# Optimization experiments

Measured on AMD Instinct MI355X. Metric: run time of the kernel, lower is better.

Reference implementation:

```python
import jax, jax.numpy as jnp
import numpy as np

NEG = 1e30  # same large negative mask constant as the torch code
E_PAIRS, N_CLASSES, SEG_LEN = 65536, 97, 8
N_ROWS = E_PAIRS * SEG_LEN


def setup_inputs() -> dict:
    key = jax.random.key(0)
    k1, k2 = jax.random.split(key)
    logits = jax.random.normal(k1, (N_ROWS, N_CLASSES), dtype=jnp.float32)
    labels = (jax.random.uniform(k2, (E_PAIRS, N_CLASSES)) < 0.05).astype(jnp.float32)
    # contiguous (st, en) ranges tiling logits rows, pos[0,0] == 0
    starts = jnp.arange(E_PAIRS, dtype=jnp.int32) * SEG_LEN
    pos = jnp.stack([starts, starts + SEG_LEN], axis=1)  # [E, 2]
    return {"logits": logits, "labels": labels, "pos": pos}


def reference(logits, labels, pos):
    E, C = labels.shape
    N = logits.shape[0]
    # pos segments are contiguous starting at pos[0,0] == 0, covering all rows
    lens = pos[:, 1] - pos[:, 0]
    seg_ids = jnp.repeat(jnp.arange(E), lens, total_repeat_length=N)  # [N]

    # ragged segment-max pooling over mention-combination rows
    e_logits = jax.ops.segment_max(logits, seg_ids, num_segments=E)  # [E, C]

    # labels[:, 0] = 0; p_mask = labels + th_label (th_label has 1 in col 0)
    labels = labels.at[:, 0].set(0.0)
    p_mask = labels.at[:, 0].set(1.0)
    n_mask = 1.0 - labels

    # loss1: masked log-softmax over pooled logits, summed over positive labels
    e_logit1 = e_logits - (1.0 - p_mask) * NEG
    loss1 = -(jax.nn.log_softmax(e_logit1, axis=-1) * labels).sum(axis=1)  # [E]

    # loss2: per-row masked log-softmax; n_mask broadcast to each row of its segment
    m_n_mask = n_mask[seg_ids]  # [N, C]
    m_logit2 = logits - (1.0 - m_n_mask) * NEG
    loss2 = -jax.nn.log_softmax(m_logit2, axis=-1)[:, 0]  # th_label selects col 0

    return loss1.mean() + loss2.mean()
```

## Files before the change

kernel.cpp:

```cpp
#include <hip/hip_runtime.h>
#include <math.h>


#define NCLS 97
#define SEGS_PER_WAVE 8
#define WAVES_PER_BLOCK 4

__global__ __launch_bounds__(256) void atloss_stage1(
    const float* __restrict__ logits,
    const float* __restrict__ labels,
    const int*   __restrict__ pos,
    float*       __restrict__ partials,
    int E, float invE, float invN)
{
    const int tid  = threadIdx.x;
    const int wv   = tid >> 6;
    const int lane = tid & 63;
    const int j    = lane & 15;
    const int r    = lane >> 4;
    const int gwave = blockIdx.x * WAVES_PER_BLOCK + wv;

    float acc1 = 0.0f;
    float acc2 = 0.0f;

    #pragma unroll 1
    for (int s = 0; s < SEGS_PER_WAVE; ++s) {
        const int e = gwave * SEGS_PER_WAVE + s;
        if (e < E) {
            const int st = pos[2 * e];
            const float* __restrict__ la = logits + (size_t)(st + r) * NCLS;
            const float* __restrict__ lb = logits + (size_t)(st + r + 4) * NCLS;
            const float* __restrict__ lg = labels + (size_t)e * NCLS;

            unsigned long long mlo = __ballot(lg[lane] > 0.5f) & ~1ull;
            unsigned long long mhi = __ballot((lane < NCLS - 64) ? (lg[64 + lane] > 0.5f)
                                                                 : false);

            float xa[7], xb[7];
            #pragma unroll
            for (int k = 0; k < 6; ++k) {
                xa[k] = la[j + 16 * k];
                xb[k] = lb[j + 16 * k];
            }
            if (j == 0) { xa[6] = la[96]; xb[6] = lb[96]; }
            else        { xa[6] = -INFINITY; xb[6] = -INFINITY; }

            float s2a = 0.0f, s2b = 0.0f;
            float cm[7];
            #pragma unroll
            for (int k = 0; k < 7; ++k) {
                const int c = j + 16 * k;
                const bool pf = (c < 64) ? ((mlo >> c) & 1ull)
                                         : ((mhi >> (c - 64)) & 1ull);
                s2a += pf ? 0.0f : __expf(xa[k]);
                s2b += pf ? 0.0f : __expf(xb[k]);
                cm[k] = fmaxf(xa[k], xb[k]);
            }
            s2a += __shfl_xor(s2a, 1); s2b += __shfl_xor(s2b, 1);
            s2a += __shfl_xor(s2a, 2); s2b += __shfl_xor(s2b, 2);
            s2a += __shfl_xor(s2a, 4); s2b += __shfl_xor(s2b, 4);
            s2a += __shfl_xor(s2a, 8); s2b += __shfl_xor(s2b, 8);
            if (j == 0)
                acc2 += (__logf(s2a) - xa[0]) + (__logf(s2b) - xb[0]);

            #pragma unroll
            for (int k = 0; k < 7; ++k) {
                cm[k] = fmaxf(cm[k], __shfl_xor(cm[k], 16));
                cm[k] = fmaxf(cm[k], __shfl_xor(cm[k], 32));
            }

            float s1 = 0.0f, psum = 0.0f;
            #pragma unroll
            for (int k = 0; k < 7; ++k) {
                const int c = j + 16 * k;
                const bool pf = (c < 64) ? ((mlo >> c) & 1ull)
                                         : ((mhi >> (c - 64)) & 1ull);
                const bool inP = pf || (c == 0);
                s1   += inP ? __expf(cm[k]) : 0.0f;
                psum += pf ? cm[k] : 0.0f;
            }
            s1   += __shfl_xor(s1, 1);   psum += __shfl_xor(psum, 1);
            s1   += __shfl_xor(s1, 2);   psum += __shfl_xor(psum, 2);
            s1   += __shfl_xor(s1, 4);   psum += __shfl_xor(psum, 4);
            s1   += __shfl_xor(s1, 8);   psum += __shfl_xor(psum, 8);
            if (lane == 0) {
                const float pcnt = (float)(__popcll(mlo) + __popcll(mhi));
                acc1 += pcnt * __logf(s1) - psum;
            }
        }
    }

    float tot = acc1 * invE + acc2 * invN;
    tot += __shfl_xor(tot, 16);
    tot += __shfl_xor(tot, 32);

    __shared__ float red[WAVES_PER_BLOCK];
    if (lane == 0) red[wv] = tot;
    __syncthreads();
    if (tid == 0) {
        float b = 0.0f;
        #pragma unroll
        for (int w = 0; w < WAVES_PER_BLOCK; ++w) b += red[w];
        partials[blockIdx.x] = b;
    }
}

__global__ __launch_bounds__(256) void atloss_reduce(
    const float* __restrict__ p, int n, float* __restrict__ out)
{
    float s = 0.0f;
    for (int i = threadIdx.x; i < n; i += 256) s += p[i];
    #pragma unroll
    for (int m = 1; m <= 32; m <<= 1) s += __shfl_xor(s, m);
    __shared__ float red[4];
    if ((threadIdx.x & 63) == 0) red[threadIdx.x >> 6] = s;
    __syncthreads();
    if (threadIdx.x == 0) out[0] = red[0] + red[1] + red[2] + red[3];
}

extern "C" void kernel_launch(void* const* d_in, const int* in_sizes, int n_in,
                              void* d_out, int out_size, void* d_ws, size_t ws_size,
                              hipStream_t stream)
{
    const float* logits = (const float*)d_in[0];
    const float* labels = (const float*)d_in[1];
    const int*   pos    = (const int*)d_in[2];

    const int E     = in_sizes[1] / NCLS;
    const int Nrows = in_sizes[0] / NCLS;

    const int segs_per_block = SEGS_PER_WAVE * WAVES_PER_BLOCK;
    const int nblocks = (E + segs_per_block - 1) / segs_per_block;

    float* partials = (float*)d_ws;

    atloss_stage1<<<nblocks, 256, 0, stream>>>(
        logits, labels, pos, partials, E, 1.0f / (float)E, 1.0f / (float)Nrows);
    atloss_reduce<<<1, 256, 0, stream>>>(partials, nblocks, (float*)d_out);
}
```

Measured before the change: 302.7 us.

## Double-buffer segment loads with register prefetch and batched pos loads

Loads all eight segment start offsets for a wave in one vector load and broadcasts them by shuffle. The per-segment loop becomes a fully unrolled software pipeline: the logits and labels loads for the next segment are issued before the current segment is computed, using two register buffers. This is meant to hide global memory latency in a bandwidth-bound kernel. It raises register pressure and loads out of range for tail segments, which are masked by clamped indices and a validity flag.

```diff
diff --git a/kernel.cpp b/kernel.cpp
--- a/kernel.cpp
+++ b/kernel.cpp
@@ -20,75 +20,103 @@
     const int r    = lane >> 4;
     const int gwave = blockIdx.x * WAVES_PER_BLOCK + wv;
 
+    int ep0 = gwave * SEGS_PER_WAVE + (lane & 7);
+    if (ep0 > E - 1) ep0 = E - 1;
+    const int stl = pos[2 * ep0];
+
     float acc1 = 0.0f;
     float acc2 = 0.0f;
 
-    #pragma unroll 1
-    for (int s = 0; s < SEGS_PER_WAVE; ++s) {
-        const int e = gwave * SEGS_PER_WAVE + s;
-        if (e < E) {
-            const int st = pos[2 * e];
-            const float* __restrict__ la = logits + (size_t)(st + r) * NCLS;
-            const float* __restrict__ lb = logits + (size_t)(st + r + 4) * NCLS;
-            const float* __restrict__ lg = labels + (size_t)e * NCLS;
+    float xaA[7], xbA[7], l0A, l1A;
+    float xaB[7], xbB[7], l0B, l1B;
 
-            unsigned long long mlo = __ballot(lg[lane] > 0.5f) & ~1ull;
-            unsigned long long mhi = __ballot((lane < NCLS - 64) ? (lg[64 + lane] > 0.5f)
-                                                                 : false);
+#define ISSUE(S, XA, XB, L0, L1)                                           \
+    do {                                                                   \
+        const int e_ = gwave * SEGS_PER_WAVE + (S);                        \
+        const int st_ = __shfl(stl, (S));                                  \
+        const float* __restrict__ la_ = logits + (size_t)(st_ + r) * NCLS; \
+        const float* __restrict__ lb_ = la_ + 4 * NCLS;                    \
+        const float* __restrict__ lg_ =                                    \
+            labels + (size_t)(e_ < E ? e_ : 0) * NCLS;                     \
+        _Pragma("unroll")                                                  \
+        for (int k = 0; k < 6; ++k) {                                      \
+            XA[k] = la_[j + 16 * k];                                       \
+            XB[k] = lb_[j + 16 * k];                                       \
+        }                                                                  \
+        XA[6] = la_[96];        \
+        XB[6] = lb_[96];                                                   \
+        L0 = lg_[lane];                                                    \
+        L1 = (lane < NCLS - 64) ? lg_[64 + lane] : 0.0f;                   \
+    } while (0)
 
-            float xa[7], xb[7];
-            #pragma unroll
-            for (int k = 0; k < 6; ++k) {
-                xa[k] = la[j + 16 * k];
-                xb[k] = lb[j + 16 * k];
-            }
-            if (j == 0) { xa[6] = la[96]; xb[6] = lb[96]; }
-            else        { xa[6] = -INFINITY; xb[6] = -INFINITY; }
+#define COMPUTE(S, XA, XB, L0, L1)                                         \
+    do {                                                                   \
+        const bool valid_ = (gwave * SEGS_PER_WAVE + (S)) < E;             \
+           \
+        unsigned long long mlo_ = __ballot(L0 > 0.5f) & ~1ull;             \
+        unsigned long long mhi_ = __ballot(L1 > 0.5f);                     \
+        float va[7], vb[7];                                                \
+        _Pragma("unroll")                                                  \
+        for (int k = 0; k < 6; ++k) { va[k] = XA[k]; vb[k] = XB[k]; }      \
+        va[6] = (j == 0) ? XA[6] : -INFINITY;                              \
+        vb[6] = (j == 0) ? XB[6] : -INFINITY;                              \
+              \
+        float s2a = 0.0f, s2b = 0.0f;                                      \
+        float cm[7];                                                       \
+        _Pragma("unroll")                                                  \
+        for (int k = 0; k < 7; ++k) {                                      \
+            const int c = j + 16 * k;                                      \
+            const bool pf = (c < 64) ? ((mlo_ >> c) & 1ull)                \
+                                     : ((mhi_ >> (c - 64)) & 1ull);        \
+            s2a += pf ? 0.0f : __expf(va[k]);                              \
+            s2b += pf ? 0.0f : __expf(vb[k]);                              \
+            cm[k] = fmaxf(va[k], vb[k]);                                   \
+        }                                                                  \
+        s2a += __shfl_xor(s2a, 1); s2b += __shfl_xor(s2b, 1);              \
+        s2a += __shfl_xor(s2a, 2); s2b += __shfl_xor(s2b, 2);              \
+        s2a += __shfl_xor(s2a, 4); s2b += __shfl_xor(s2b, 4);              \
+        s2a += __shfl_xor(s2a, 8); s2b += __shfl_xor(s2b, 8);              \
+        if (j == 0 && valid_)                                              \
+            acc2 += (__logf(s2a) - va[0]) + (__logf(s2b) - vb[0]);         \
+                      \
+        _Pragma("unroll")                                                  \
+        for (int k = 0; k < 7; ++k) {                                      \
+            cm[k] = fmaxf(cm[k], __shfl_xor(cm[k], 16));                   \
+            cm[k] = fmaxf(cm[k], __shfl_xor(cm[k], 32));                   \
+        }                                                                  \
+             \
+        float s1 = 0.0f, psum = 0.0f;                                      \
+        _Pragma("unroll")                                                  \
+        for (int k = 0; k < 7; ++k) {                                      \
+            const int c = j + 16 * k;                                      \
+            const bool pf = (c < 64) ? ((mlo_ >> c) & 1ull)                \
+                                     : ((mhi_ >> (c - 64)) & 1ull);        \
+            const bool inP = pf || (c == 0);                               \
+            s1   += inP ? __expf(cm[k]) : 0.0f;                            \
+            psum += pf ? cm[k] : 0.0f;                                     \
+        }                                                                  \
+        s1 += __shfl_xor(s1, 1);  psum += __shfl_xor(psum, 1);             \
+        s1 += __shfl_xor(s1, 2);  psum += __shfl_xor(psum, 2);             \
+        s1 += __shfl_xor(s1, 4);  psum += __shfl_xor(psum, 4);             \
+        s1 += __shfl_xor(s1, 8);  psum += __shfl_xor(psum, 8);             \
+        if (lane == 0 && valid_) {                                         \
+            const float pcnt = (float)(__popcll(mlo_) + __popcll(mhi_));   \
+            acc1 += pcnt * __logf(s1) - psum;                              \
+        }                                                                  \
+    } while (0)
 
-            float s2a = 0.0f, s2b = 0.0f;
-            float cm[7];
-            #pragma unroll
-            for (int k = 0; k < 7; ++k) {
-                const int c = j + 16 * k;
-                const bool pf = (c < 64) ? ((mlo >> c) & 1ull)
-                                         : ((mhi >> (c - 64)) & 1ull);
-                s2a += pf ? 0.0f : __expf(xa[k]);
-                s2b += pf ? 0.0f : __expf(xb[k]);
-                cm[k] = fmaxf(xa[k], xb[k]);
-            }
-            s2a += __shfl_xor(s2a, 1); s2b += __shfl_xor(s2b, 1);
-            s2a += __shfl_xor(s2a, 2); s2b += __shfl_xor(s2b, 2);
-            s2a += __shfl_xor(s2a, 4); s2b += __shfl_xor(s2b, 4);
-            s2a += __shfl_xor(s2a, 8); s2b += __shfl_xor(s2b, 8);
-            if (j == 0)
-                acc2 += (__logf(s2a) - xa[0]) + (__logf(s2b) - xb[0]);
+    ISSUE(0, xaA, xbA, l0A, l1A);
+    #pragma unroll
+    for (int s = 0; s < SEGS_PER_WAVE; s += 2) {
+        ISSUE(s + 1, xaB, xbB, l0B, l1B);
+        COMPUTE(s, xaA, xbA, l0A, l1A);
+        if (s + 2 < SEGS_PER_WAVE)
+            ISSUE(s + 2, xaA, xbA, l0A, l1A);
+        COMPUTE(s + 1, xaB, xbB, l0B, l1B);
+    }
 
-            #pragma unroll
-            for (int k = 0; k < 7; ++k) {
-                cm[k] = fmaxf(cm[k], __shfl_xor(cm[k], 16));
-                cm[k] = fmaxf(cm[k], __shfl_xor(cm[k], 32));
-            }
-
-            float s1 = 0.0f, psum = 0.0f;
-            #pragma unroll
-            for (int k = 0; k < 7; ++k) {
-                const int c = j + 16 * k;
-                const bool pf = (c < 64) ? ((mlo >> c) & 1ull)
-                                         : ((mhi >> (c - 64)) & 1ull);
-                const bool inP = pf || (c == 0);
-                s1   += inP ? __expf(cm[k]) : 0.0f;
-                psum += pf ? cm[k] : 0.0f;
-            }
-            s1   += __shfl_xor(s1, 1);   psum += __shfl_xor(psum, 1);
-            s1   += __shfl_xor(s1, 2);   psum += __shfl_xor(psum, 2);
-            s1   += __shfl_xor(s1, 4);   psum += __shfl_xor(psum, 4);
-            s1   += __shfl_xor(s1, 8);   psum += __shfl_xor(psum, 8);
-            if (lane == 0) {
-                const float pcnt = (float)(__popcll(mlo) + __popcll(mhi));
-                acc1 += pcnt * __logf(s1) - psum;
-            }
-        }
-    }
+#undef ISSUE
+#undef COMPUTE
 
     float tot = acc1 * invE + acc2 * invN;
     tot += __shfl_xor(tot, 16);
```

Result: no change. 304.4 us (+0.5%).
